# Performance work log

Hardware: AMD Instinct MI355X
Metric: run time of the kernel (lower is better)

## Reference

```python
import jax, jax.numpy as jnp
import numpy as np

N, C, H = 4096, 768, 12
HD = C // H
SCALE = HD ** -0.5


def setup_inputs() -> dict:
    key = jax.random.key(0)
    k1, k2, k3 = jax.random.split(key, 3)
    x = jax.random.normal(k1, (N, C), dtype=jnp.float32)
    w_qkv = jax.random.normal(k2, (C, 3 * C), dtype=jnp.float32) * (C ** -0.5)
    w_proj = jax.random.normal(k3, (C, C), dtype=jnp.float32) * (C ** -0.5)
    b_proj = jnp.zeros((C,), dtype=jnp.float32)
    return {"x": x, "w_qkv": w_qkv, "w_proj": w_proj, "b_proj": b_proj}


def reference(x, w_qkv, w_proj, b_proj):
    n, c = x.shape
    # fused QKV projection (qkv_bias=False): [N, 3C] -> [3, H, N, hd]
    qkv = (x @ w_qkv).reshape(n, 3, H, HD)
    qkv = jnp.transpose(qkv, (1, 2, 0, 3))  # (3, H, N, hd)
    q, k, v = qkv[0], qkv[1], qkv[2]
    # scaled dot-product attention per head: (H, N, N)
    attn = jnp.einsum('hnd,hmd->hnm', q, k) * SCALE
    attn = jax.nn.softmax(attn, axis=-1)
    # attn_drop is identity (rate=0, eval mode)
    out = jnp.einsum('hnm,hmd->hnd', attn, v)          # (H, N, hd)
    out = jnp.transpose(out, (1, 0, 2)).reshape(n, c)  # (N, C)
    # output projection (bias by default in nn.Dense); proj_drop identity
    return out @ w_proj + b_proj
```

## Files before the change

### kernel.cpp

```cpp
#include <hip/hip_runtime.h>

#define N_TOK 4096
#define C_DIM 768
#define H_NUM 12
#define QKV_N 2304

typedef __attribute__((ext_vector_type(8))) short bf16x8;
typedef __attribute__((ext_vector_type(4))) float f32x4;
typedef __attribute__((ext_vector_type(16))) float f32x16;
typedef __attribute__((ext_vector_type(4))) unsigned int u32x4;

static __device__ __forceinline__ unsigned short f2bf(float f) {
  unsigned u = __builtin_bit_cast(unsigned, f);
  u += 0x7FFF + ((u >> 16) & 1);
  return (unsigned short)(u >> 16);
}

static __device__ __forceinline__ float bf2f(unsigned short u) {
  return __builtin_bit_cast(float, (unsigned)u << 16);
}

static __device__ __forceinline__ float exp2_fast(float x) {
  float r; asm("v_exp_f32 %0, %1" : "=v"(r) : "v"(x)); return r;
}

#define GLOAD_LDS16(g, l)                                                     \
  __builtin_amdgcn_global_load_lds(                                           \
      (const __attribute__((address_space(1))) void*)(g),                     \
      (__attribute__((address_space(3))) void*)(l), 16, 0, 0)

#define Q_SCALE 0.18033688011112042f

__global__ __launch_bounds__(256) void conv_bf16(
    const float* __restrict__ in, unsigned short* __restrict__ out, int n8) {
  const int i = blockIdx.x * 256 + threadIdx.x;
  if (i >= n8) return;
  const float4 a = reinterpret_cast<const float4*>(in)[i * 2];
  const float4 b = reinterpret_cast<const float4*>(in)[i * 2 + 1];
  unsigned short tmp[8] = {f2bf(a.x), f2bf(a.y), f2bf(a.z), f2bf(a.w),
                           f2bf(b.x), f2bf(b.y), f2bf(b.z), f2bf(b.w)};
  reinterpret_cast<bf16x8*>(out)[i] = *reinterpret_cast<bf16x8*>(tmp);
}

__global__ __launch_bounds__(256) void transpose_cvt(
    const float* __restrict__ in, unsigned short* __restrict__ out,
    int K, int N) {
  __shared__ unsigned short T[64][65];
  const int t = threadIdx.x;
  const int k0 = blockIdx.y * 64, n0 = blockIdx.x * 64;
  {
    const int r = t >> 2, qd = t & 3;
#pragma unroll
    for (int i = 0; i < 4; ++i) {
      const int c = qd * 16 + i * 4;
      const float4 v = *reinterpret_cast<const float4*>(
          &in[(size_t)(k0 + r) * N + n0 + c]);
      T[r][c + 0] = f2bf(v.x); T[r][c + 1] = f2bf(v.y);
      T[r][c + 2] = f2bf(v.z); T[r][c + 3] = f2bf(v.w);
    }
  }
  __syncthreads();
#pragma unroll
  for (int i = 0; i < 2; ++i) {
    const int cid = t + i * 256;
    const int rn = cid >> 3, cx = cid & 7;
    unsigned short tmp[8];
#pragma unroll
    for (int j = 0; j < 8; ++j) tmp[j] = T[cx * 8 + j][rn];
    *reinterpret_cast<bf16x8*>(&out[(size_t)(n0 + rn) * K + k0 + cx * 8]) =
        *reinterpret_cast<bf16x8*>(tmp);
  }
}

__global__ __launch_bounds__(256) void gemm_qkv_bf16(
    const unsigned short* __restrict__ A, const unsigned short* __restrict__ Bt,
    unsigned short* __restrict__ qw, unsigned short* __restrict__ kw,
    unsigned short* __restrict__ vw) {
  __shared__ unsigned short As[128 * 32];
  __shared__ unsigned short Bs[128 * 32];
  const int t = threadIdx.x;
  const int lane = t & 63, wid = t >> 6;
  const int lr = lane & 15, lg = lane >> 4;
  const int lid = blockIdx.y * 18 + blockIdx.x;
  const int swz = (lid & 7) * 72 + (lid >> 3);
  const int m_base = (swz / 18) * 128, n_base = (swz % 18) * 128;
  const int wm = (wid >> 1) * 64, wn = (wid & 1) * 64;
  const int c_row = lane >> 2;
  const int c_col = (lane & 3) * 8;

  f32x4 acc[4][4];
#pragma unroll
  for (int mt = 0; mt < 4; ++mt)
#pragma unroll
    for (int nt = 0; nt < 4; ++nt) acc[mt][nt] = (f32x4){0.f, 0.f, 0.f, 0.f};

  for (int kt = 0; kt < 24; ++kt) {
    const int k0 = kt * 32;
    __syncthreads();
#pragma unroll
    for (int i = 0; i < 2; ++i) {
      const int ch = wid * 2 + i;
      GLOAD_LDS16(&A[(size_t)(m_base + ch * 16 + c_row) * 768 + k0 + c_col],
                  &As[ch * 512]);
      GLOAD_LDS16(&Bt[(size_t)(n_base + ch * 16 + c_row) * 768 + k0 + c_col],
                  &Bs[ch * 512]);
    }
    __syncthreads();
    bf16x8 af[4], bfr[4];
#pragma unroll
    for (int mt = 0; mt < 4; ++mt)
      af[mt] = *reinterpret_cast<const bf16x8*>(&As[(wm + mt * 16 + lr) * 32 + lg * 8]);
#pragma unroll
    for (int nt = 0; nt < 4; ++nt)
      bfr[nt] = *reinterpret_cast<const bf16x8*>(&Bs[(wn + nt * 16 + lr) * 32 + lg * 8]);
#pragma unroll
    for (int mt = 0; mt < 4; ++mt)
#pragma unroll
      for (int nt = 0; nt < 4; ++nt)
        acc[mt][nt] = __builtin_amdgcn_mfma_f32_16x16x32_bf16(af[mt], bfr[nt],
                                                              acc[mt][nt], 0, 0, 0);
  }
#pragma unroll
  for (int mt = 0; mt < 4; ++mt)
#pragma unroll
    for (int nt = 0; nt < 4; ++nt)
#pragma unroll
      for (int r = 0; r < 4; ++r) {
        const int m = m_base + wm + mt * 16 + lg * 4 + r;
        const int c = n_base + wn + nt * 16 + lr;
        const float v = acc[mt][nt][r];
        const int which = c / 768;
        const int cc = c - which * 768;
        const int h = cc >> 6, d = cc & 63;
        if (which == 0) {
          qw[((size_t)h * N_TOK + m) * 64 + d] = f2bf(v * Q_SCALE);
        } else if (which == 1) {
          kw[((size_t)h * N_TOK + m) * 64 + d] = f2bf(v);
        } else {
          vw[((size_t)h * 64 + d) * N_TOK + m] = f2bf(v);
        }
      }
}

__global__ __launch_bounds__(256) void gemm_proj_bf16(
    const unsigned short* __restrict__ A, const unsigned short* __restrict__ Bt,
    const float* __restrict__ bias, float* __restrict__ out) {
  __shared__ unsigned short As[128 * 32];
  __shared__ unsigned short Bs[128 * 32];
  const int t = threadIdx.x;
  const int lane = t & 63, wid = t >> 6;
  const int lr = lane & 15, lg = lane >> 4;
  const int lid = blockIdx.y * 6 + blockIdx.x;
  const int swz = (lid & 7) * 24 + (lid >> 3);
  const int m_base = (swz / 6) * 128, n_base = (swz % 6) * 128;
  const int wm = (wid >> 1) * 64, wn = (wid & 1) * 64;
  const int c_row = lane >> 2;
  const int c_col = (lane & 3) * 8;

  f32x4 acc[4][4];
#pragma unroll
  for (int mt = 0; mt < 4; ++mt)
#pragma unroll
    for (int nt = 0; nt < 4; ++nt) acc[mt][nt] = (f32x4){0.f, 0.f, 0.f, 0.f};

  for (int kt = 0; kt < 24; ++kt) {
    const int k0 = kt * 32;
    __syncthreads();
#pragma unroll
    for (int i = 0; i < 2; ++i) {
      const int ch = wid * 2 + i;
      GLOAD_LDS16(&A[(size_t)(m_base + ch * 16 + c_row) * 768 + k0 + c_col],
                  &As[ch * 512]);
      GLOAD_LDS16(&Bt[(size_t)(n_base + ch * 16 + c_row) * 768 + k0 + c_col],
                  &Bs[ch * 512]);
    }
    __syncthreads();
    bf16x8 af[4], bfr[4];
#pragma unroll
    for (int mt = 0; mt < 4; ++mt)
      af[mt] = *reinterpret_cast<const bf16x8*>(&As[(wm + mt * 16 + lr) * 32 + lg * 8]);
#pragma unroll
    for (int nt = 0; nt < 4; ++nt)
      bfr[nt] = *reinterpret_cast<const bf16x8*>(&Bs[(wn + nt * 16 + lr) * 32 + lg * 8]);
#pragma unroll
    for (int mt = 0; mt < 4; ++mt)
#pragma unroll
      for (int nt = 0; nt < 4; ++nt)
        acc[mt][nt] = __builtin_amdgcn_mfma_f32_16x16x32_bf16(af[mt], bfr[nt],
                                                              acc[mt][nt], 0, 0, 0);
  }
#pragma unroll
  for (int nt = 0; nt < 4; ++nt) {
    const int n = n_base + wn + nt * 16 + lr;
    const float bv = bias[n];
#pragma unroll
    for (int mt = 0; mt < 4; ++mt)
#pragma unroll
      for (int r = 0; r < 4; ++r) {
        const int m = m_base + wm + mt * 16 + lg * 4 + r;
        out[(size_t)m * 768 + n] = acc[mt][nt][r] + bv;
      }
  }
}

__global__ __launch_bounds__(256) void attn_kernel(
    const unsigned short* __restrict__ qw, const unsigned short* __restrict__ kw,
    const unsigned short* __restrict__ vw, unsigned short* __restrict__ po0,
    unsigned short* __restrict__ po1, float* __restrict__ lw) {
  __shared__ unsigned short smem[18432];
  const int t = threadIdx.x;
  const int lane = t & 63;
  const int wid = t >> 6;
  const int qsub = wid & 1;
  const int kvh = wid >> 1;
  const int q31 = lane & 31;
  const int hi = lane >> 5;
  const int swz = (blockIdx.x & 7) * 192 + (blockIdx.x >> 3);
  const int h = swz >> 7;
  const int rem = swz & 127;
  const int half = rem >> 6;
  const int qt = rem & 63;
  const int q0 = qt * 64 + qsub * 32;

  unsigned short* Ks = &smem[kvh * 9216];
  unsigned short* Vs = Ks + 4608;

  const unsigned short* kbase = &kw[(size_t)h * N_TOK * 64];
  const unsigned short* vbase = &vw[(size_t)h * 64 * N_TOK];
  const int kv0 = half * 2048 + kvh * 1024;

  bf16x8 qf[4];
#pragma unroll
  for (int ks = 0; ks < 4; ++ks)
    qf[ks] = *reinterpret_cast<const bf16x8*>(
        &qw[((size_t)h * N_TOK + q0 + q31) * 64 + ks * 16 + hi * 8]);

  f32x16 acc0, acc1;
#pragma unroll
  for (int r = 0; r < 16; ++r) { acc0[r] = 0.f; acc1[r] = 0.f; }
  float l_run = 0.f;

  const int tg = t & 127;
  const int srow = tg >> 3;
  const int sseg = (tg & 7) * 8;

  bf16x8 kst[4], vst[4];
#pragma unroll
  for (int i = 0; i < 4; ++i) {
    const int row = srow + i * 16;
    kst[i] = *reinterpret_cast<const bf16x8*>(&kbase[(size_t)(kv0 + row) * 64 + sseg]);
    vst[i] = *reinterpret_cast<const bf16x8*>(&vbase[(size_t)row * N_TOK + kv0 + sseg]);
  }

  for (int kvt = 0; kvt < 16; ++kvt) {
    const int kv = kv0 + kvt * 64;
    __syncthreads();
#pragma unroll
    for (int i = 0; i < 4; ++i) {
      const int row = srow + i * 16;
      *reinterpret_cast<bf16x8*>(&Ks[row * 72 + sseg]) = kst[i];
      *reinterpret_cast<bf16x8*>(&Vs[row * 72 + sseg]) = vst[i];
    }
    __syncthreads();
    const int kvn = (kvt + 1 < 16) ? kv + 64 : kv0;
#pragma unroll
    for (int i = 0; i < 4; ++i) {
      const int row = srow + i * 16;
      kst[i] = *reinterpret_cast<const bf16x8*>(&kbase[(size_t)(kvn + row) * 64 + sseg]);
      vst[i] = *reinterpret_cast<const bf16x8*>(&vbase[(size_t)row * N_TOK + kvn + sseg]);
    }

#pragma unroll
    for (int ct = 0; ct < 2; ++ct) {
      f32x16 s;
#pragma unroll
      for (int r = 0; r < 16; ++r) s[r] = 0.f;
      __builtin_amdgcn_s_setprio(1);
#pragma unroll
      for (int ks = 0; ks < 4; ++ks) {
        const bf16x8 kf = *reinterpret_cast<const bf16x8*>(
            &Ks[(ct * 32 + q31) * 72 + ks * 16 + hi * 8]);
        s = __builtin_amdgcn_mfma_f32_32x32x16_bf16(kf, qf[ks], s, 0, 0, 0);
      }
      __builtin_amdgcn_s_setprio(0);

      float p[16];
#pragma unroll
      for (int r = 0; r < 16; ++r) p[r] = exp2_fast(s[r]);
      float s8[8];
#pragma unroll
      for (int r = 0; r < 8; ++r) s8[r] = p[r] + p[r + 8];
#pragma unroll
      for (int r = 0; r < 4; ++r) s8[r] = s8[r] + s8[r + 4];
      l_run += (s8[0] + s8[1]) + (s8[2] + s8[3]);

      unsigned dw[8];
#pragma unroll
      for (int m2 = 0; m2 < 8; ++m2)
        asm("v_cvt_pk_bf16_f32 %0, %1, %2"
            : "=v"(dw[m2]) : "v"(p[2 * m2]), "v"(p[2 * m2 + 1]));
      asm("v_permlane32_swap_b32 %0, %1" : "+v"(dw[0]), "+v"(dw[2]));
      asm("v_permlane32_swap_b32 %0, %1" : "+v"(dw[1]), "+v"(dw[3]));
      asm("v_permlane32_swap_b32 %0, %1" : "+v"(dw[4]), "+v"(dw[6]));
      asm("v_permlane32_swap_b32 %0, %1" : "+v"(dw[5]), "+v"(dw[7]));

      __builtin_amdgcn_s_setprio(1);
#pragma unroll
      for (int ksl = 0; ksl < 2; ++ksl) {
        u32x4 u;
        u.x = dw[ksl * 4 + 0]; u.y = dw[ksl * 4 + 1];
        u.z = dw[ksl * 4 + 2]; u.w = dw[ksl * 4 + 3];
        const bf16x8 pa = __builtin_bit_cast(bf16x8, u);
        const int kg = ct * 2 + ksl;
        const bf16x8 vf0 = *reinterpret_cast<const bf16x8*>(
            &Vs[q31 * 72 + kg * 16 + hi * 8]);
        const bf16x8 vf1 = *reinterpret_cast<const bf16x8*>(
            &Vs[(32 + q31) * 72 + kg * 16 + hi * 8]);
        acc0 = __builtin_amdgcn_mfma_f32_32x32x16_bf16(pa, vf0, acc0, 0, 0, 0);
        acc1 = __builtin_amdgcn_mfma_f32_32x32x16_bf16(pa, vf1, acc1, 0, 0, 0);
      }
      __builtin_amdgcn_s_setprio(0);
    }
  }

  l_run += __shfl_xor(l_run, 32);

  __syncthreads();
  float* ex = reinterpret_cast<float*>(smem) + qsub * 2304;
  if (kvh == 1) {
    float* pdst = ex + lane * 36;
#pragma unroll
    for (int r = 0; r < 16; ++r) { pdst[r] = acc0[r]; pdst[16 + r] = acc1[r]; }
    pdst[32] = l_run;
  }
  __syncthreads();
  if (kvh == 0) {
    const float* psrc = ex + lane * 36;
    const float lt = l_run + psrc[32];
    const float linv = 1.0f / lt;
    unsigned short* pout = half ? po1 : po0;
#pragma unroll
    for (int r = 0; r < 16; ++r) {
      const int crow = (r & 3) + 8 * (r >> 2) + 4 * hi;
      const float iv = __shfl(linv, crow);
      const size_t base = (size_t)(q0 + crow) * C_DIM + h * 64;
      pout[base + q31] = f2bf((acc0[r] + psrc[r]) * iv);
      pout[base + 32 + q31] = f2bf((acc1[r] + psrc[16 + r]) * iv);
    }
    if (hi == 0) lw[half * 49152 + h * 4096 + q0 + q31] = lt;
  }
}

__global__ __launch_bounds__(256) void attn_merge(
    unsigned short* __restrict__ po0, const unsigned short* __restrict__ po1,
    const float* __restrict__ lw) {
  const int i = blockIdx.x * 256 + threadIdx.x;
  const int base = i * 8;
  const int q = base / 768;
  const int c = base - q * 768;
  const int h = c >> 6;
  const float l0 = lw[h * 4096 + q];
  const float l1 = lw[49152 + h * 4096 + q];
  const float w = 1.0f / (l0 + l1);
  const float w0 = l0 * w, w1 = l1 * w;
  const bf16x8 a = *reinterpret_cast<const bf16x8*>(&po0[base]);
  const bf16x8 b = *reinterpret_cast<const bf16x8*>(&po1[base]);
  unsigned short tmp[8];
#pragma unroll
  for (int j = 0; j < 8; ++j)
    tmp[j] = f2bf(w0 * bf2f((unsigned short)a[j]) +
                  w1 * bf2f((unsigned short)b[j]));
  *reinterpret_cast<bf16x8*>(&po0[base]) = *reinterpret_cast<bf16x8*>(tmp);
}

extern "C" void kernel_launch(void* const* d_in, const int* in_sizes, int n_in,
                              void* d_out, int out_size, void* d_ws, size_t ws_size,
                              hipStream_t stream) {
  (void)in_sizes; (void)n_in; (void)out_size; (void)ws_size;
  const float* x = (const float*)d_in[0];
  const float* w_qkv = (const float*)d_in[1];
  const float* w_proj = (const float*)d_in[2];
  const float* b_proj = (const float*)d_in[3];
  float* out = (float*)d_out;

  const size_t HNd = (size_t)H_NUM * N_TOK * 64;
  unsigned short* qw = (unsigned short*)d_ws;
  unsigned short* kw = qw + HNd;
  unsigned short* vw = kw + HNd;
  unsigned short* xb = vw + HNd;
  unsigned short* ow = xb;
  unsigned short* wT = xb + HNd;
  unsigned short* wqkvT = wT;
  unsigned short* wprojT = wT;
  unsigned short* po1 = wT + HNd;
  float* lw = (float*)(po1 + HNd);

  conv_bf16<<<dim3((N_TOK * C_DIM / 8 + 255) / 256), 256, 0, stream>>>(
      x, xb, N_TOK * C_DIM / 8);
  transpose_cvt<<<dim3(QKV_N / 64, C_DIM / 64), 256, 0, stream>>>(
      w_qkv, wqkvT, C_DIM, QKV_N);
  gemm_qkv_bf16<<<dim3(QKV_N / 128, N_TOK / 128), 256, 0, stream>>>(
      xb, wqkvT, qw, kw, vw);
  transpose_cvt<<<dim3(C_DIM / 64, C_DIM / 64), 256, 0, stream>>>(
      w_proj, wprojT, C_DIM, C_DIM);
  attn_kernel<<<dim3(1536), 256, 0, stream>>>(qw, kw, vw, ow, po1, lw);
  attn_merge<<<dim3(N_TOK * C_DIM / 8 / 256), 256, 0, stream>>>(ow, po1, lw);
  gemm_proj_bf16<<<dim3(C_DIM / 128, N_TOK / 128), 256, 0, stream>>>(
      ow, wprojT, b_proj, out);
}
```

Baseline: 152.5 us.

## Give each attention block 128 queries sharing one KV stream instead of intra-block KV split

The attention block previously split its KV range across two wave pairs and merged their partial accumulators through shared memory. Now all four waves process distinct 32-query slices over the same full 2048-key half, so each K/V tile loaded into shared memory is reused by 128 queries instead of 64. This halves the block count, halves LDS use, and removes the in-block merge and its extra barriers. In exchange each block runs twice as many KV iterations and the grid of 768 blocks gives less parallelism.

New measurement: 141.5 us. 7.2% less time.

```diff
diff --git a/kernel.cpp b/kernel.cpp
--- a/kernel.cpp
+++ b/kernel.cpp
@@ -207,27 +207,25 @@
     const unsigned short* __restrict__ qw, const unsigned short* __restrict__ kw,
     const unsigned short* __restrict__ vw, unsigned short* __restrict__ po0,
     unsigned short* __restrict__ po1, float* __restrict__ lw) {
-  __shared__ unsigned short smem[18432];
+  __shared__ unsigned short smem[9216];
   const int t = threadIdx.x;
   const int lane = t & 63;
-  const int wid = t >> 6;
-  const int qsub = wid & 1;
-  const int kvh = wid >> 1;
+  const int qsub = t >> 6;
   const int q31 = lane & 31;
   const int hi = lane >> 5;
-  const int swz = (blockIdx.x & 7) * 192 + (blockIdx.x >> 3);
-  const int h = swz >> 7;
-  const int rem = swz & 127;
-  const int half = rem >> 6;
-  const int qt = rem & 63;
-  const int q0 = qt * 64 + qsub * 32;
-
-  unsigned short* Ks = &smem[kvh * 9216];
-  unsigned short* Vs = Ks + 4608;
+  const int swz = (blockIdx.x & 7) * 96 + (blockIdx.x >> 3);
+  const int h = swz >> 6;
+  const int rem = swz & 63;
+  const int half = rem >> 5;
+  const int qst = rem & 31;
+  const int q0 = qst * 128 + qsub * 32;
+
+  unsigned short* Ks = smem;
+  unsigned short* Vs = smem + 4608;
 
   const unsigned short* kbase = &kw[(size_t)h * N_TOK * 64];
   const unsigned short* vbase = &vw[(size_t)h * 64 * N_TOK];
-  const int kv0 = half * 2048 + kvh * 1024;
+  const int kv0 = half * 2048;
 
   bf16x8 qf[4];
 #pragma unroll
@@ -240,35 +238,31 @@
   for (int r = 0; r < 16; ++r) { acc0[r] = 0.f; acc1[r] = 0.f; }
   float l_run = 0.f;
 
-  const int tg = t & 127;
-  const int srow = tg >> 3;
-  const int sseg = (tg & 7) * 8;
-
-  bf16x8 kst[4], vst[4];
-#pragma unroll
-  for (int i = 0; i < 4; ++i) {
-    const int row = srow + i * 16;
-    kst[i] = *reinterpret_cast<const bf16x8*>(&kbase[(size_t)(kv0 + row) * 64 + sseg]);
-    vst[i] = *reinterpret_cast<const bf16x8*>(&vbase[(size_t)row * N_TOK + kv0 + sseg]);
-  }
-
-  for (int kvt = 0; kvt < 16; ++kvt) {
+  const int srow0 = t >> 3;
+  const int srow1 = (t + 256) >> 3;
+  const int sseg = (t & 7) * 8;
+
+  bf16x8 kst[2], vst[2];
+  {
+    kst[0] = *reinterpret_cast<const bf16x8*>(&kbase[(size_t)(kv0 + srow0) * 64 + sseg]);
+    kst[1] = *reinterpret_cast<const bf16x8*>(&kbase[(size_t)(kv0 + srow1) * 64 + sseg]);
+    vst[0] = *reinterpret_cast<const bf16x8*>(&vbase[(size_t)srow0 * N_TOK + kv0 + sseg]);
+    vst[1] = *reinterpret_cast<const bf16x8*>(&vbase[(size_t)srow1 * N_TOK + kv0 + sseg]);
+  }
+
+  for (int kvt = 0; kvt < 32; ++kvt) {
     const int kv = kv0 + kvt * 64;
     __syncthreads();
-#pragma unroll
-    for (int i = 0; i < 4; ++i) {
-      const int row = srow + i * 16;
-      *reinterpret_cast<bf16x8*>(&Ks[row * 72 + sseg]) = kst[i];
-      *reinterpret_cast<bf16x8*>(&Vs[row * 72 + sseg]) = vst[i];
-    }
-    __syncthreads();
-    const int kvn = (kvt + 1 < 16) ? kv + 64 : kv0;
-#pragma unroll
-    for (int i = 0; i < 4; ++i) {
-      const int row = srow + i * 16;
-      kst[i] = *reinterpret_cast<const bf16x8*>(&kbase[(size_t)(kvn + row) * 64 + sseg]);
-      vst[i] = *reinterpret_cast<const bf16x8*>(&vbase[(size_t)row * N_TOK + kvn + sseg]);
-    }
+    *reinterpret_cast<bf16x8*>(&Ks[srow0 * 72 + sseg]) = kst[0];
+    *reinterpret_cast<bf16x8*>(&Ks[srow1 * 72 + sseg]) = kst[1];
+    *reinterpret_cast<bf16x8*>(&Vs[srow0 * 72 + sseg]) = vst[0];
+    *reinterpret_cast<bf16x8*>(&Vs[srow1 * 72 + sseg]) = vst[1];
+    __syncthreads();
+    const int kvn = (kvt + 1 < 32) ? kv + 64 : kv0;
+    kst[0] = *reinterpret_cast<const bf16x8*>(&kbase[(size_t)(kvn + srow0) * 64 + sseg]);
+    kst[1] = *reinterpret_cast<const bf16x8*>(&kbase[(size_t)(kvn + srow1) * 64 + sseg]);
+    vst[0] = *reinterpret_cast<const bf16x8*>(&vbase[(size_t)srow0 * N_TOK + kvn + sseg]);
+    vst[1] = *reinterpret_cast<const bf16x8*>(&vbase[(size_t)srow1 * N_TOK + kvn + sseg]);
 
 #pragma unroll
     for (int ct = 0; ct < 2; ++ct) {
@@ -324,31 +318,17 @@
   }
 
   l_run += __shfl_xor(l_run, 32);
-
-  __syncthreads();
-  float* ex = reinterpret_cast<float*>(smem) + qsub * 2304;
-  if (kvh == 1) {
-    float* pdst = ex + lane * 36;
-#pragma unroll
-    for (int r = 0; r < 16; ++r) { pdst[r] = acc0[r]; pdst[16 + r] = acc1[r]; }
-    pdst[32] = l_run;
-  }
-  __syncthreads();
-  if (kvh == 0) {
-    const float* psrc = ex + lane * 36;
-    const float lt = l_run + psrc[32];
-    const float linv = 1.0f / lt;
-    unsigned short* pout = half ? po1 : po0;
-#pragma unroll
-    for (int r = 0; r < 16; ++r) {
-      const int crow = (r & 3) + 8 * (r >> 2) + 4 * hi;
-      const float iv = __shfl(linv, crow);
-      const size_t base = (size_t)(q0 + crow) * C_DIM + h * 64;
-      pout[base + q31] = f2bf((acc0[r] + psrc[r]) * iv);
-      pout[base + 32 + q31] = f2bf((acc1[r] + psrc[16 + r]) * iv);
-    }
-    if (hi == 0) lw[half * 49152 + h * 4096 + q0 + q31] = lt;
-  }
+  const float linv = 1.0f / l_run;
+  unsigned short* pout = half ? po1 : po0;
+#pragma unroll
+  for (int r = 0; r < 16; ++r) {
+    const int crow = (r & 3) + 8 * (r >> 2) + 4 * hi;
+    const float iv = __shfl(linv, crow);
+    const size_t base = (size_t)(q0 + crow) * C_DIM + h * 64;
+    pout[base + q31] = f2bf(acc0[r] * iv);
+    pout[base + 32 + q31] = f2bf(acc1[r] * iv);
+  }
+  if (hi == 0) lw[half * 49152 + h * 4096 + q0 + q31] = l_run;
 }
 
 __global__ __launch_bounds__(256) void attn_merge(
@@ -403,7 +383,7 @@
       xb, wqkvT, qw, kw, vw);
   transpose_cvt<<<dim3(C_DIM / 64, C_DIM / 64), 256, 0, stream>>>(
       w_proj, wprojT, C_DIM, C_DIM);
-  attn_kernel<<<dim3(1536), 256, 0, stream>>>(qw, kw, vw, ow, po1, lw);
+  attn_kernel<<<dim3(768), 256, 0, stream>>>(qw, kw, vw, ow, po1, lw);
   attn_merge<<<dim3(N_TOK * C_DIM / 8 / 256), 256, 0, stream>>>(ow, po1, lw);
   gemm_proj_bf16<<<dim3(C_DIM / 128, N_TOK / 128), 256, 0, stream>>>(
       ow, wprojT, b_proj, out);
```
